# Kernel optimization log

Measured on AMD Instinct MI355X. Metric: run time of the kernel, lower is better.

## Reference

```python
import jax, jax.numpy as jnp
import numpy as np

B, Z, H, D, T, L = 2048, 64, 256, 8, 250, 2


def setup_inputs() -> dict:
    key = jax.random.key(0)
    ks = jax.random.split(key, 10)
    s = 0.05  # small init scale for stable LSTM dynamics
    n = lambda k, shp, sc=1.0: jax.random.normal(k, shp, dtype=jnp.float32) * sc
    return {
        "z": n(ks[0], (B, Z)),
        "target_seq": n(ks[1], (B, T, D)),
        "fc_hidden_w": n(ks[2], (Z, H * L), s),
        "fc_hidden_b": jnp.zeros((H * L,), jnp.float32),
        "fc_cell_w": n(ks[3], (Z, H * L), s),
        "fc_cell_b": jnp.zeros((H * L,), jnp.float32),
        "W_ih0": n(ks[4], (D, 4 * H), s),
        "W_hh0": n(ks[5], (H, 4 * H), s),
        "b_ih0": jnp.zeros((4 * H,), jnp.float32),
        "b_hh0": jnp.zeros((4 * H,), jnp.float32),
        "W_ih1": n(ks[6], (H, 4 * H), s),
        "W_hh1": n(ks[7], (H, 4 * H), s),
        "b_ih1": jnp.zeros((4 * H,), jnp.float32),
        "b_hh1": jnp.zeros((4 * H,), jnp.float32),
        "fc_out_w": n(ks[8], (H, D), s),
        "fc_out_b": jnp.zeros((D,), jnp.float32),
    }


def _lstm_cell(x, h, c, Wih, Whh, bih, bhh):
    # PyTorch gate order: i, f, g, o
    gates = x @ Wih + bih + h @ Whh + bhh  # [B, 4H]
    i, f, g, o = jnp.split(gates, 4, axis=-1)
    c_new = jax.nn.sigmoid(f) * c + jax.nn.sigmoid(i) * jnp.tanh(g)
    h_new = jax.nn.sigmoid(o) * jnp.tanh(c_new)
    return h_new, c_new


def reference(z, target_seq, fc_hidden_w, fc_hidden_b, fc_cell_w, fc_cell_b,
              W_ih0, W_hh0, b_ih0, b_hh0, W_ih1, W_hh1, b_ih1, b_hh1,
              fc_out_w, fc_out_b):
    bsz = z.shape[0]
    # Faithful to torch .view(num_layers, batch, hidden) on [B, H*L] output
    h0_all = (z @ fc_hidden_w + fc_hidden_b).reshape(L, bsz, H)
    c0_all = (z @ fc_cell_w + fc_cell_b).reshape(L, bsz, H)
    # Teacher forcing ratio 1.0: input at step t is target[:, t-1] (zeros at t=0)
    first = jnp.zeros((bsz, 1, target_seq.shape[-1]), target_seq.dtype)
    inputs = jnp.concatenate([first, target_seq[:, :-1]], axis=1)  # [B, T, D]
    xs = jnp.transpose(inputs, (1, 0, 2))  # time-major [T, B, D]

    def step(carry, xt):
        h0, c0, h1, c1 = carry
        h0, c0 = _lstm_cell(xt, h0, c0, W_ih0, W_hh0, b_ih0, b_hh0)
        h1, c1 = _lstm_cell(h0, h1, c1, W_ih1, W_hh1, b_ih1, b_hh1)
        return (h0, c0, h1, c1), h1

    init = (h0_all[0], c0_all[0], h0_all[1], c0_all[1])
    _, hs = jax.lax.scan(step, init, xs)  # hs: [T, B, H]
    hs = jnp.transpose(hs, (1, 0, 2))  # [B, T, H]
    reconstructed = hs @ fc_out_w + fc_out_b  # [B, T, D]
    return reconstructed
```

## Files before the change

### kernel.cpp

```cpp
#include <hip/hip_runtime.h>
#include <cstddef>
#include <cstdint>


#define BSZ    2048
#define ZDIM   64
#define HDIM   256
#define DDIM   8
#define TSTEPS 250
#define ROWS   16
#define NWG    (BSZ / ROWS)
#define NTH    512
#define G4     1024
#define WSTR   264

typedef __attribute__((ext_vector_type(4))) int v4i;

__device__ __forceinline__ unsigned short f2bf(float x) {
  union { float f; unsigned u; } v; v.f = x;
  unsigned r = v.u + 0x7fff + ((v.u >> 16) & 1);
  return (unsigned short)(r >> 16);
}
__device__ __forceinline__ float bf2f(unsigned short b) {
  union { unsigned u; float f; } v; v.u = (unsigned)b << 16; return v.f;
}
__device__ __forceinline__ float fexp2(float x) { return __builtin_amdgcn_exp2f(x); }
__device__ __forceinline__ float frcp(float x)  { return __builtin_amdgcn_rcpf(x); }
__device__ __forceinline__ float sigm(float x)  { return frcp(1.f + fexp2(-1.44269504f * x)); }
__device__ __forceinline__ float tanh_(float x) { return 2.f * frcp(1.f + fexp2(-2.88539008f * x)) - 1.f; }
__device__ __forceinline__ char q8(float x, float s) {
  float v = fminf(fmaxf(x * s, -127.f), 127.f);
  return (char)(int)__builtin_rintf(v);
}
__device__ __forceinline__ void q8pair(float h, float s, char* hi, char* lo) {
  float hs = fminf(fmaxf(h * s, -127.f), 127.f);
  float hq = __builtin_rintf(hs);
  *hi = (char)(int)hq;
  *lo = (char)(int)__builtin_rintf((hs - hq) * 254.f);
}

__device__ __forceinline__ void async_copy16(const void* g, void* l) {
  __builtin_amdgcn_global_load_lds(
      reinterpret_cast<const __attribute__((address_space(1))) unsigned int*>(
          reinterpret_cast<uintptr_t>(g)),
      reinterpret_cast<__attribute__((address_space(3))) unsigned int*>(
          reinterpret_cast<uintptr_t>(l)),
      16, 0, 0);
}
template <int N>
__device__ __forceinline__ void wait_vmcnt() {
  __builtin_amdgcn_s_waitcnt((N & 15) | (7 << 4) | (15 << 8) | (((N >> 4) & 3) << 14));
}

__global__ void init_state(const float* __restrict__ z,
                           const float* __restrict__ Wfh, const float* __restrict__ bfh,
                           const float* __restrict__ Wfc, const float* __restrict__ bfc,
                           char* __restrict__ h0h, char* __restrict__ h0l,
                           char* __restrict__ h1h, char* __restrict__ h1l,
                           float* __restrict__ c0s, float* __restrict__ c1s)
{
  int idx = blockIdx.x * 256 + threadIdx.x;
  int b = idx >> 8;
  int j = idx & 255;
  int col = ((b & 1) << 8) | j;
  const float* z0 = z + (size_t)(b >> 1) * ZDIM;
  const float* z1 = z + (size_t)(1024 + (b >> 1)) * ZDIM;
  float h0 = bfh[col], c0v = bfc[col], h1 = bfh[col], c1v = bfc[col];
  for (int k = 0; k < ZDIM; ++k) {
    float wh = Wfh[k * 512 + col];
    float wc = Wfc[k * 512 + col];
    float a = z0[k], bb = z1[k];
    h0  += a * wh;  c0v += a * wc;
    h1  += bb * wh; c1v += bb * wc;
  }
  char hi, lo;
  q8pair(h0, 31.75f, &hi, &lo); h0h[idx] = hi; h0l[idx] = lo;
  q8pair(h1, 31.75f, &hi, &lo); h1h[idx] = hi; h1l[idx] = lo;
  c0s[idx] = c0v; c1s[idx] = c1v;
}

__global__ void col_scales(const float* __restrict__ Whh0,
                           const float* __restrict__ Wih1, const float* __restrict__ Whh1,
                           float* __restrict__ cs0, float* __restrict__ qs0,
                           float* __restrict__ cs1, float* __restrict__ qs1)
{
  int c = blockIdx.x * 256 + threadIdx.x;
  if (c < 1024) {
    float m = 0.f;
    for (int k = 0; k < 256; ++k) m = fmaxf(m, fabsf(Whh0[(size_t)k * G4 + c]));
    cs0[c] = m * (1.f / 16129.f);
    qs0[c] = 127.f / m;
  } else {
    c -= 1024;
    float m = 0.f;
    for (int k = 0; k < 256; ++k) m = fmaxf(m, fabsf(Whh1[(size_t)k * G4 + c]));
    for (int k = 0; k < 256; ++k) m = fmaxf(m, fabsf(Wih1[(size_t)k * G4 + c]));
    cs1[c] = m * (1.f / 16129.f);
    qs1[c] = 127.f / m;
  }
}

__global__ void pack_i8(const float* __restrict__ Whh0,
                        const float* __restrict__ Wih1, const float* __restrict__ Whh1,
                        const float* __restrict__ qs0, const float* __restrict__ qs1,
                        char* __restrict__ p0, char* __restrict__ p1)
{
  int tt   = blockIdx.x * 4 + (threadIdx.x >> 6);
  int lane = threadIdx.x & 63;
  int l15 = lane & 15, lq = lane >> 4;
  union { char c[16]; uint4 u; } v;
  if (tt < 256) {
    int w = tt >> 5, kc = (tt >> 3) & 3, i = tt & 7;
    int nt = (i >> 1) * 16 + 2 * w + (i & 1);
    int col = nt * 16 + l15;
    float q = qs0[col];
    for (int j = 0; j < 16; ++j) {
      int k = kc * 64 + lq * 16 + j;
      v.c[j] = q8(Whh0[(size_t)k * G4 + col], q);
    }
    *(uint4*)(p0 + (size_t)tt * 1024 + lane * 16) = v.u;
  } else {
    int t1 = tt - 256;
    int w = t1 >> 6, kc = (t1 >> 3) & 7, i = t1 & 7;
    int nt = (i >> 1) * 16 + 2 * w + (i & 1);
    int col = nt * 16 + l15;
    float q = qs1[col];
    for (int j = 0; j < 16; ++j) {
      int k = kc * 64 + lq * 16 + j;
      float wv = (k < 256) ? Whh1[(size_t)k * G4 + col]
                           : Wih1[(size_t)(k - 256) * G4 + col];
      v.c[j] = q8(wv, q);
    }
    *(uint4*)(p1 + (size_t)t1 * 1024 + lane * 16) = v.u;
  }
}

__global__ __launch_bounds__(NTH, 1) void lstm_run(
    const float* __restrict__ target,
    const char* __restrict__ p0, const char* __restrict__ p1,
    const float* __restrict__ bih0, const float* __restrict__ bhh0,
    const float* __restrict__ bih1, const float* __restrict__ bhh1,
    const float* __restrict__ Wih0,
    const float* __restrict__ Wout, const float* __restrict__ bout,
    const char* __restrict__ h0h, const char* __restrict__ h0l,
    const char* __restrict__ h1h, const char* __restrict__ h1l,
    const float* __restrict__ c0s, const float* __restrict__ c1s,
    const float* __restrict__ cs0, const float* __restrict__ cs1,
    float* __restrict__ out)
{
  __shared__ uint4 ring[8][4][64];
  __shared__ uint4 X4h[32 * 16];
  __shared__ uint4 X4l[32 * 16];
  __shared__ unsigned short h1f[16 * WSTR];
  __shared__ unsigned short woutT[8 * WSTR];
  __shared__ float x_lds[16 * 8];

  const int tid  = threadIdx.x;
  const int w    = tid >> 6;
  const int lane = tid & 63;
  const int l15  = lane & 15;
  const int lq   = lane >> 4;
  const int b0   = blockIdx.x * ROWS;
  char* Xch = (char*)X4h;
  char* Xcl = (char*)X4l;

  {
    int m = tid & 15, blk = tid >> 4;
    const char* sh = (blk < 16) ? h1h : h0h;
    const char* sl = (blk < 16) ? h1l : h0l;
    int jblk = blk & 15;
    X4h[blk * 16 + m] = *(const uint4*)(sh + (size_t)(b0 + m) * HDIM + jblk * 16);
    X4l[blk * 16 + m] = *(const uint4*)(sl + (size_t)(b0 + m) * HDIM + jblk * 16);
  }
  for (int i = tid; i < HDIM * DDIM; i += NTH) {
    int k = i >> 3, d = i & 7;
    woutT[d * WSTR + k] = f2bf(Wout[i]);
  }

  const int myrow = lq * 4;
  const int jc0   = 32 * w + l15;
  float c0r[2][4], c1r[2][4];
  float bA0[8], bA1[8], csA0[8], csA1[8];
  float wx[8][8];
#pragma unroll
  for (int i = 0; i < 8; ++i) {
    int col = (i >> 1) * 256 + jc0 + 16 * (i & 1);
    bA0[i]  = bih0[col] + bhh0[col];
    bA1[i]  = bih1[col] + bhh1[col];
    csA0[i] = cs0[col];
    csA1[i] = cs1[col];
#pragma unroll
    for (int d = 0; d < 8; ++d) wx[i][d] = Wih0[d * G4 + col];
  }
#pragma unroll
  for (int cc = 0; cc < 2; ++cc) {
    int j = jc0 + cc * 16;
#pragma unroll
    for (int r = 0; r < 4; ++r) {
      c0r[cc][r] = c0s[(size_t)(b0 + myrow + r) * HDIM + j];
      c1r[cc][r] = c1s[(size_t)(b0 + myrow + r) * HDIM + j];
    }
  }
  const int opr = tid >> 5, opd = (tid >> 2) & 7, opq = tid & 3;
  const float bo_out = bout[opd];

  const char* gp0 = p0 + (size_t)w * 32768 + lane * 16;
  const char* gp1 = p1 + (size_t)w * 65536 + lane * 16;

#define A0VH(KC) __builtin_bit_cast(v4i, X4h[(16 + (KC) * 4 + lq) * 16 + l15])
#define A0VL(KC) __builtin_bit_cast(v4i, X4l[(16 + (KC) * 4 + lq) * 16 + l15])
#define A1VH(KC) __builtin_bit_cast(v4i, X4h[((KC) * 4 + lq) * 16 + l15])
#define A1VL(KC) __builtin_bit_cast(v4i, X4l[((KC) * 4 + lq) * 16 + l15])

  async_copy16(gp0,        &ring[w][0][0]);
  async_copy16(gp0 + 1024, &ring[w][1][0]);
  async_copy16(gp0 + 2048, &ring[w][2][0]);
  async_copy16(gp0 + 3072, &ring[w][3][0]);

  __syncthreads();

#pragma unroll 1
  for (int t = 0; t < TSTEPS; ++t) {
    if (tid < 128) {
      int m = tid >> 3, d = tid & 7;
      x_lds[m * 8 + d] = (t == 0) ? 0.f
          : target[(size_t)(b0 + m) * (TSTEPS * DDIM) + (size_t)(t - 1) * DDIM + d];
    }
    __syncthreads();

    const float sc0 = (t <= 1) ? 4.f : 1.f;
    const float sc1 = (t == 0) ? 4.f : 1.f;
    const float wq0 = (t == 0) ? 31.75f : 127.f;

    v4i acch[8], accl[8];
    const v4i zi = {0, 0, 0, 0};

#pragma unroll
    for (int i = 0; i < 8; ++i) { acch[i] = zi; accl[i] = zi; }
    {
      v4i ah, al;
#pragma unroll 8
      for (int j = 0; j < 32; ++j) {
        const int i = j & 7, s = j & 3;
        if (i == 0) { int kc = j >> 3; ah = A0VH(kc); al = A0VL(kc); }
        wait_vmcnt<3>();
        v4i bb = __builtin_bit_cast(v4i, ring[w][s][lane]);
        acch[i] = __builtin_amdgcn_mfma_i32_16x16x64_i8(ah, bb, acch[i], 0, 0, 0);
        accl[i] = __builtin_amdgcn_mfma_i32_16x16x64_i8(al, bb, accl[i], 0, 0, 0);
        const int jn = j + 4;
        if (jn < 32) async_copy16(gp0 + (size_t)jn * 1024, &ring[w][s][0]);
        else         async_copy16(gp1 + (size_t)(jn - 32) * 1024, &ring[w][s][0]);
      }
    }
    __syncthreads();

    {
      float4 xa[4], xb[4];
#pragma unroll
      for (int r = 0; r < 4; ++r) {
        xa[r] = *(const float4*)&x_lds[(myrow + r) * 8];
        xb[r] = *(const float4*)&x_lds[(myrow + r) * 8 + 4];
      }
#pragma unroll
      for (int cc = 0; cc < 2; ++cc) {
        float gf4[4][4];
#pragma unroll
        for (int g = 0; g < 4; ++g) {
          int i = g * 2 + cc;
          float cs = csA0[i] * sc0;
#pragma unroll
          for (int r = 0; r < 4; ++r)
            gf4[g][r] = ((float)acch[i][r] + (float)accl[i][r] * (1.f / 254.f)) * cs + bA0[i];
        }
#pragma unroll
        for (int g = 0; g < 4; ++g) {
          int i = g * 2 + cc;
#pragma unroll
          for (int r = 0; r < 4; ++r)
            gf4[g][r] += xa[r].x * wx[i][0] + xa[r].y * wx[i][1]
                       + xa[r].z * wx[i][2] + xa[r].w * wx[i][3]
                       + xb[r].x * wx[i][4] + xb[r].y * wx[i][5]
                       + xb[r].z * wx[i][6] + xb[r].w * wx[i][7];
        }
#pragma unroll
        for (int r = 0; r < 4; ++r) {
          float iv = sigm(gf4[0][r]);
          float fv = sigm(gf4[1][r]);
          float gv = tanh_(gf4[2][r]);
          float ov = sigm(gf4[3][r]);
          c0r[cc][r] = fv * c0r[cc][r] + iv * gv;
          char hi, lo;
          q8pair(ov * tanh_(c0r[cc][r]), wq0, &hi, &lo);
          int off = ((16 + 2 * w + cc) * 16 + myrow + r) * 16 + l15;
          Xch[off] = hi; Xcl[off] = lo;
        }
      }
    }
    __syncthreads();

#pragma unroll
    for (int i = 0; i < 8; ++i) { acch[i] = zi; accl[i] = zi; }
    {
      v4i ah, al;
#pragma unroll 8
      for (int j = 0; j < 64; ++j) {
        const int i = j & 7, s = j & 3;
        if (i == 0) { int kc = j >> 3; ah = A1VH(kc); al = A1VL(kc); }
        wait_vmcnt<3>();
        v4i bb = __builtin_bit_cast(v4i, ring[w][s][lane]);
        acch[i] = __builtin_amdgcn_mfma_i32_16x16x64_i8(ah, bb, acch[i], 0, 0, 0);
        accl[i] = __builtin_amdgcn_mfma_i32_16x16x64_i8(al, bb, accl[i], 0, 0, 0);
        const int jn = j + 4;
        if (jn < 64) async_copy16(gp1 + (size_t)jn * 1024, &ring[w][s][0]);
        else         async_copy16(gp0 + (size_t)(jn - 64) * 1024, &ring[w][s][0]);
      }
    }
    __syncthreads();

#pragma unroll
    for (int cc = 0; cc < 2; ++cc)
#pragma unroll
      for (int r = 0; r < 4; ++r) {
        float di = ((float)acch[0 + cc][r] + (float)accl[0 + cc][r] * (1.f / 254.f));
        float df = ((float)acch[2 + cc][r] + (float)accl[2 + cc][r] * (1.f / 254.f));
        float dg = ((float)acch[4 + cc][r] + (float)accl[4 + cc][r] * (1.f / 254.f));
        float dv = ((float)acch[6 + cc][r] + (float)accl[6 + cc][r] * (1.f / 254.f));
        float iv = sigm(di * csA1[0 + cc] * sc1 + bA1[0 + cc]);
        float fv = sigm(df * csA1[2 + cc] * sc1 + bA1[2 + cc]);
        float gv = tanh_(dg * csA1[4 + cc] * sc1 + bA1[4 + cc]);
        float ov = sigm(dv * csA1[6 + cc] * sc1 + bA1[6 + cc]);
        c1r[cc][r] = fv * c1r[cc][r] + iv * gv;
        float h = ov * tanh_(c1r[cc][r]);
        char hi, lo;
        q8pair(h, 127.f, &hi, &lo);
        int off = ((2 * w + cc) * 16 + myrow + r) * 16 + l15;
        Xch[off] = hi; Xcl[off] = lo;
        h1f[(myrow + r) * WSTR + jc0 + cc * 16] = f2bf(h);
      }
    __syncthreads();

    {
      float s_ = 0.f;
#pragma unroll
      for (int i = 0; i < 16; ++i) {
        ushort4 hx = *(const ushort4*)&h1f[opr * WSTR + i * 16 + opq * 4];
        ushort4 wv = *(const ushort4*)&woutT[opd * WSTR + i * 16 + opq * 4];
        s_ += bf2f(hx.x) * bf2f(wv.x) + bf2f(hx.y) * bf2f(wv.y)
            + bf2f(hx.z) * bf2f(wv.z) + bf2f(hx.w) * bf2f(wv.w);
      }
      s_ += __shfl_xor(s_, 1);
      s_ += __shfl_xor(s_, 2);
      if (opq == 0)
        out[(size_t)(b0 + opr) * (TSTEPS * DDIM) + (size_t)t * DDIM + opd] =
            s_ + bo_out;
    }
  }
#undef A0VH
#undef A0VL
#undef A1VH
#undef A1VL
}

extern "C" void kernel_launch(void* const* d_in, const int* in_sizes, int n_in,
                              void* d_out, int out_size, void* d_ws, size_t ws_size,
                              hipStream_t stream) {
  const float* z    = (const float*)d_in[0];
  const float* tgt  = (const float*)d_in[1];
  const float* Wfh  = (const float*)d_in[2];
  const float* bfh  = (const float*)d_in[3];
  const float* Wfc  = (const float*)d_in[4];
  const float* bfc  = (const float*)d_in[5];
  const float* Wih0 = (const float*)d_in[6];
  const float* Whh0 = (const float*)d_in[7];
  const float* bih0 = (const float*)d_in[8];
  const float* bhh0 = (const float*)d_in[9];
  const float* Wih1 = (const float*)d_in[10];
  const float* Whh1 = (const float*)d_in[11];
  const float* bih1 = (const float*)d_in[12];
  const float* bhh1 = (const float*)d_in[13];
  const float* Wout = (const float*)d_in[14];
  const float* bout = (const float*)d_in[15];

  char* ws = (char*)d_ws;
  char*  p0   = ws;
  char*  p1   = ws + 262144;
  char*  h0h  = ws + 786432;
  char*  h0l  = ws + 1310720;
  char*  h1h  = ws + 1835008;
  char*  h1l  = ws + 2359296;
  float* c0s  = (float*)(ws + 2883584);
  float* c1s  = (float*)(ws + 4980736);
  float* cs0  = (float*)(ws + 7077888);
  float* qs0  = (float*)(ws + 7081984);
  float* cs1  = (float*)(ws + 7086080);
  float* qs1  = (float*)(ws + 7090176);

  hipLaunchKernelGGL(init_state, dim3(BSZ * HDIM / 256), dim3(256), 0, stream,
                     z, Wfh, bfh, Wfc, bfc, h0h, h0l, h1h, h1l, c0s, c1s);
  hipLaunchKernelGGL(col_scales, dim3(8), dim3(256), 0, stream,
                     Whh0, Wih1, Whh1, cs0, qs0, cs1, qs1);
  hipLaunchKernelGGL(pack_i8, dim3(192), dim3(256), 0, stream,
                     Whh0, Wih1, Whh1, qs0, qs1, p0, p1);
  hipLaunchKernelGGL(lstm_run, dim3(NWG), dim3(NTH), 0, stream,
                     tgt, p0, p1, bih0, bhh0, bih1, bhh1, Wih0, Wout, bout,
                     h0h, h0l, h1h, h1l, c0s, c1s, cs0, cs1, (float*)d_out);
}
```

Baseline: 3.055 ms.

## Double-buffer layer-0 hidden state to drop per-step barriers and reuse quantized h1

Layer-0 hidden state now ping-pongs between two LDS slots selected by timestep parity, so the barrier between the layer-0 MFMA loop and the layer-0 gate writes can be removed. The next step's target input load moves to the end of the step, removing the barrier at loop start. The output projection reads the int8 hi/lo quantized h1 already in LDS instead of a separate bf16 copy, which removes the h1f array and its stores. In exchange it adds a dequantization in the output dot product, a larger X buffer, and a reliance on double-buffering to stay race-free.

```diff
diff --git a/kernel.cpp b/kernel.cpp
--- a/kernel.cpp
+++ b/kernel.cpp
@@ -149,9 +149,8 @@
     float* __restrict__ out)
 {
   __shared__ uint4 ring[8][4][64];
-  __shared__ uint4 X4h[32 * 16];
-  __shared__ uint4 X4l[32 * 16];
-  __shared__ unsigned short h1f[16 * WSTR];
+  __shared__ uint4 X4h[48 * 16];
+  __shared__ uint4 X4l[48 * 16];
   __shared__ unsigned short woutT[8 * WSTR];
   __shared__ float x_lds[16 * 8];
 
@@ -176,6 +175,7 @@
     int k = i >> 3, d = i & 7;
     woutT[d * WSTR + k] = f2bf(Wout[i]);
   }
+  if (tid < 128) x_lds[tid] = 0.f;
 
   const int myrow = lq * 4;
   const int jc0   = 32 * w + l15;
@@ -207,10 +207,12 @@
   const char* gp0 = p0 + (size_t)w * 32768 + lane * 16;
   const char* gp1 = p1 + (size_t)w * 65536 + lane * 16;
 
-#define A0VH(KC) __builtin_bit_cast(v4i, X4h[(16 + (KC) * 4 + lq) * 16 + l15])
-#define A0VL(KC) __builtin_bit_cast(v4i, X4l[(16 + (KC) * 4 + lq) * 16 + l15])
-#define A1VH(KC) __builtin_bit_cast(v4i, X4h[((KC) * 4 + lq) * 16 + l15])
-#define A1VL(KC) __builtin_bit_cast(v4i, X4l[((KC) * 4 + lq) * 16 + l15])
+#define A0VH(KC) __builtin_bit_cast(v4i, X4h[(pb0 + (KC) * 4 + lq) * 16 + l15])
+#define A0VL(KC) __builtin_bit_cast(v4i, X4l[(pb0 + (KC) * 4 + lq) * 16 + l15])
+#define A1VH(KC) __builtin_bit_cast(v4i, \
+    X4h[(((KC) < 4 ? (KC) * 4 : pb1 + ((KC) - 4) * 4) + lq) * 16 + l15])
+#define A1VL(KC) __builtin_bit_cast(v4i, \
+    X4l[(((KC) < 4 ? (KC) * 4 : pb1 + ((KC) - 4) * 4) + lq) * 16 + l15])
 
   async_copy16(gp0,        &ring[w][0][0]);
   async_copy16(gp0 + 1024, &ring[w][1][0]);
@@ -221,13 +223,8 @@
 
 #pragma unroll 1
   for (int t = 0; t < TSTEPS; ++t) {
-    if (tid < 128) {
-      int m = tid >> 3, d = tid & 7;
-      x_lds[m * 8 + d] = (t == 0) ? 0.f
-          : target[(size_t)(b0 + m) * (TSTEPS * DDIM) + (size_t)(t - 1) * DDIM + d];
-    }
-    __syncthreads();
-
+    const int pb0 = 16 + ((t & 1) << 4);
+    const int pb1 = 48 - pb0;
     const float sc0 = (t <= 1) ? 4.f : 1.f;
     const float sc1 = (t == 0) ? 4.f : 1.f;
     const float wq0 = (t == 0) ? 31.75f : 127.f;
@@ -252,7 +249,6 @@
         else         async_copy16(gp1 + (size_t)(jn - 32) * 1024, &ring[w][s][0]);
       }
     }
-    __syncthreads();
 
     {
       float4 xa[4], xb[4];
@@ -291,7 +287,7 @@
           c0r[cc][r] = fv * c0r[cc][r] + iv * gv;
           char hi, lo;
           q8pair(ov * tanh_(c0r[cc][r]), wq0, &hi, &lo);
-          int off = ((16 + 2 * w + cc) * 16 + myrow + r) * 16 + l15;
+          int off = ((pb1 + 2 * w + cc) * 16 + myrow + r) * 16 + l15;
           Xch[off] = hi; Xcl[off] = lo;
         }
       }
@@ -335,24 +331,36 @@
         q8pair(h, 127.f, &hi, &lo);
         int off = ((2 * w + cc) * 16 + myrow + r) * 16 + l15;
         Xch[off] = hi; Xcl[off] = lo;
-        h1f[(myrow + r) * WSTR + jc0 + cc * 16] = f2bf(h);
-      }
+      }
+
+    if (tid < 128) {
+      int m = tid >> 3, d = tid & 7;
+      x_lds[m * 8 + d] =
+          target[(size_t)(b0 + m) * (TSTEPS * DDIM) + (size_t)t * DDIM + d];
+    }
     __syncthreads();
 
     {
       float s_ = 0.f;
 #pragma unroll
       for (int i = 0; i < 16; ++i) {
-        ushort4 hx = *(const ushort4*)&h1f[opr * WSTR + i * 16 + opq * 4];
+        int off = (i * 16 + opr) * 16 + opq * 4;
+        int hb = *(const int*)(Xch + off);
+        int lb = *(const int*)(Xcl + off);
         ushort4 wv = *(const ushort4*)&woutT[opd * WSTR + i * 16 + opq * 4];
-        s_ += bf2f(hx.x) * bf2f(wv.x) + bf2f(hx.y) * bf2f(wv.y)
-            + bf2f(hx.z) * bf2f(wv.z) + bf2f(hx.w) * bf2f(wv.w);
+        const unsigned short* wp = (const unsigned short*)&wv;
+#pragma unroll
+        for (int q = 0; q < 4; ++q) {
+          float hv = (float)((char)(hb >> (8 * q)))
+                   + (float)((char)(lb >> (8 * q))) * (1.f / 254.f);
+          s_ += hv * bf2f(wp[q]);
+        }
       }
       s_ += __shfl_xor(s_, 1);
       s_ += __shfl_xor(s_, 2);
       if (opq == 0)
         out[(size_t)(b0 + opr) * (TSTEPS * DDIM) + (size_t)t * DDIM + opd] =
-            s_ + bo_out;
+            s_ * (1.f / 127.f) + bo_out;
     }
   }
 #undef A0VH
```

After: 3.179 ms. +4.0%, slower.
